# Optimization experiments

Hardware: AMD Instinct MI355X
Metric: run time of the kernel (lower is better)

Reference implementation:

```python
import jax, jax.numpy as jnp
import numpy as np

B, T, D = 4, 4096, 1024
HD = 64              # head_dim
H = D // HD          # n_heads = 16
C = 64               # chunk_size (T % C == 0)


def setup_inputs() -> dict:
    key = jax.random.key(0)
    k1, k2, k3 = jax.random.split(key, 3)
    out = jax.random.normal(k1, (B, T, D), jnp.float32)
    # Linear(d_model, d_model, bias=False) weights, ~1/sqrt(D) scale
    W_write = jax.random.normal(k2, (D, D), jnp.float32) * 0.03
    W_read = jax.random.normal(k3, (D, D), jnp.float32) * 0.03
    decay = jnp.full((H,), 4.6, jnp.float32)                 # torch init value
    log_alpha = jnp.log(jnp.full((H,), 0.03, jnp.float32))   # memory_alpha=0.03
    return {"out": out, "W_write": W_write, "W_read": W_read,
            "decay": decay, "log_alpha": log_alpha}


def reference(out, W_write, W_read, decay, log_alpha):
    Bb, Tt, Dd = out.shape
    d, Hh, Cc = HD, D // HD, C
    out32 = out.astype(jnp.float32)
    gamma = jax.nn.sigmoid(decay)          # (H,)
    log_gamma = jnp.log(gamma)

    # projections and head split: (B, H, T, d)
    v = (out32 @ W_write.T).reshape(Bb, Tt, Hh, d).transpose(0, 2, 1, 3)
    rk = out32.reshape(Bb, Tt, Hh, d).transpose(0, 2, 1, 3)
    wk = jnp.pad(rk[:, :, :-1], ((0, 0), (0, 0), (1, 0), (0, 0)))  # shift right by 1

    BH = Bb * Hh
    gamma_bh = jnp.tile(gamma, Bb)          # (BH,) index b*H+h -> gamma[h]
    log_gamma_bh = jnp.tile(log_gamma, Bb)
    nC = Tt // Cc
    # (nC, BH, C, d) so lax.scan runs over chunks
    v_ch = v.reshape(BH, nC, Cc, d).transpose(1, 0, 2, 3)
    rk_ch = rk.reshape(BH, nC, Cc, d).transpose(1, 0, 2, 3)
    wk_ch = wk.reshape(BH, nC, Cc, d).transpose(1, 0, 2, 3)

    p = jnp.arange(Cc)
    diffs = jnp.clip(p[:, None] - 1 - p[None, :], 0)          # (C, C)
    causal = p[:, None] > p[None, :]
    # per-(b,h) intra-chunk decay mask (BH, C, C)
    M = jnp.exp(diffs[None].astype(jnp.float32) * log_gamma_bh[:, None, None]) * causal[None]
    g_p = gamma_bh[:, None] ** p[None, :].astype(jnp.float32)            # (BH, C)
    g_w = gamma_bh[:, None] ** (Cc - 1 - p)[None, :].astype(jnp.float32)  # (BH, C)
    g_C = gamma_bh ** Cc                                                  # (BH,)

    def scan_fn(W, chunk):
        rk_c, wk_c, v_c = chunk                                   # each (BH, C, d)
        inter = jnp.einsum('bij,bcj->bci', W, rk_c) * g_p[:, :, None]
        S = jnp.einsum('bcd,bkd->bck', rk_c, wk_c)                # (BH, C, C)
        intra = jnp.einsum('bck,bkd->bcd', S * M, v_c)
        W_new = g_C[:, None, None] * W + jnp.einsum('bci,bcj->bij', v_c * g_w[:, :, None], wk_c)
        return W_new, inter + intra

    W0 = jnp.zeros((BH, d, d), jnp.float32)
    _, reads = jax.lax.scan(scan_fn, W0, (rk_ch, wk_ch, v_ch))   # (nC, BH, C, d)
    reads = reads.transpose(1, 0, 2, 3).reshape(Bb, Hh, Tt, d)
    alpha = jnp.exp(log_alpha)[None, :, None, None]
    reads = (alpha * reads).transpose(0, 2, 1, 3).reshape(Bb, Tt, Dd)
    return out + (reads @ W_read.T).astype(out.dtype)
```

## Files before the change

### kernel.cpp

```cpp
#include <hip/hip_runtime.h>
#include <hip/hip_bf16.h>
#include <stdint.h>


typedef __bf16 bf16x8 __attribute__((ext_vector_type(8)));
typedef float f32x4 __attribute__((ext_vector_type(4)));

#define GAS __attribute__((address_space(1)))
#define LAS __attribute__((address_space(3)))

__device__ __forceinline__ unsigned short f2bf(float f) {
  unsigned u = __float_as_uint(f);
  u = (u + 0x7fffu + ((u >> 16) & 1u)) >> 16;
  return (unsigned short)u;
}
__device__ __forceinline__ float bf2f(unsigned short h) {
  return __uint_as_float(((unsigned)h) << 16);
}

__global__ __launch_bounds__(256) void cast_f32_to_bf16(
    const float* __restrict__ src, unsigned short* __restrict__ dst, int n8) {
  int i = blockIdx.x * 256 + threadIdx.x;
  if (i >= n8) return;
  const float4* s = (const float4*)src + (size_t)i * 2;
  float4 f0 = s[0], f1 = s[1];
  union { uint4 u4; unsigned short us[8]; } o;
  o.us[0] = f2bf(f0.x); o.us[1] = f2bf(f0.y); o.us[2] = f2bf(f0.z); o.us[3] = f2bf(f0.w);
  o.us[4] = f2bf(f1.x); o.us[5] = f2bf(f1.y); o.us[6] = f2bf(f1.z); o.us[7] = f2bf(f1.w);
  ((uint4*)dst)[i] = o.u4;
}

__global__ __launch_bounds__(256) void cast_weights(
    const float* __restrict__ w1, const float* __restrict__ w2,
    unsigned short* __restrict__ dst) {
  int i = blockIdx.x * 256 + threadIdx.x;
  const float* src = (i < 131072) ? w1 : w2;
  int j = (i < 131072) ? i : i - 131072;
  const float4* s = (const float4*)src + (size_t)j * 2;
  float4 f0 = s[0], f1 = s[1];
  union { uint4 u4; unsigned short us[8]; } o;
  o.us[0] = f2bf(f0.x); o.us[1] = f2bf(f0.y); o.us[2] = f2bf(f0.z); o.us[3] = f2bf(f0.w);
  o.us[4] = f2bf(f1.x); o.us[5] = f2bf(f1.y); o.us[6] = f2bf(f1.z); o.us[7] = f2bf(f1.w);
  ((uint4*)dst)[i] = o.u4;
}

__device__ __forceinline__ void swizzle_bm_bn(int id, int& bm, int& bn) {
  int x = id & 7;
  int s = id >> 3;
  bn = s & 7;
  bm = ((s >> 3) << 3) | x;
}

__global__ __launch_bounds__(256, 4) void gemm_bt_bf16out(
    const unsigned short* __restrict__ A, const unsigned short* __restrict__ B,
    unsigned short* __restrict__ C, int M, int N, int K) {
  __shared__ unsigned short As[2][128 * 32];
  __shared__ unsigned short Bs[2][128 * 32];
  int tid = threadIdx.x;
  int l = tid & 63, w = tid >> 6;
  int bm, bn;
  swizzle_bm_bn(blockIdx.x, bm, bn);
  int wm = (w >> 1) * 64, wn = (w & 1) * 64;
  f32x4 acc[4][4];
#pragma unroll
  for (int mi = 0; mi < 4; mi++)
#pragma unroll
    for (int ni = 0; ni < 4; ni++) acc[mi][ni] = (f32x4){0.f, 0.f, 0.f, 0.f};
  const unsigned short* Ab = A + (size_t)bm * 128 * K;
  const unsigned short* Bb = B + (size_t)bn * 128 * K;
  int lr = l >> 2, lc = (l & 3) * 8;
  int lm = l & 15, q4 = l >> 4;
  const int nit = K >> 5;
#pragma unroll
  for (int q = 0; q < 2; q++) {
    int g = (w * 2 + q) * 16 + lr;
    __builtin_amdgcn_global_load_lds((GAS void*)(void*)(Ab + (size_t)g * K + lc),
                                     (LAS void*)(&As[0][(w * 2 + q) * 512]), 16, 0, 0);
    __builtin_amdgcn_global_load_lds((GAS void*)(void*)(Bb + (size_t)g * K + lc),
                                     (LAS void*)(&Bs[0][(w * 2 + q) * 512]), 16, 0, 0);
  }
  for (int it = 0; it < nit; it++) {
    __syncthreads();
    int buf = it & 1;
    if (it + 1 < nit) {
      int k0 = (it + 1) << 5;
#pragma unroll
      for (int q = 0; q < 2; q++) {
        int g = (w * 2 + q) * 16 + lr;
        __builtin_amdgcn_global_load_lds((GAS void*)(void*)(Ab + (size_t)g * K + k0 + lc),
                                         (LAS void*)(&As[buf ^ 1][(w * 2 + q) * 512]), 16, 0, 0);
        __builtin_amdgcn_global_load_lds((GAS void*)(void*)(Bb + (size_t)g * K + k0 + lc),
                                         (LAS void*)(&Bs[buf ^ 1][(w * 2 + q) * 512]), 16, 0, 0);
      }
    }
    bf16x8 a[4], b[4];
#pragma unroll
    for (int mi = 0; mi < 4; mi++) a[mi] = *(const bf16x8*)&As[buf][(wm + mi * 16 + lm) * 32 + q4 * 8];
#pragma unroll
    for (int ni = 0; ni < 4; ni++) b[ni] = *(const bf16x8*)&Bs[buf][(wn + ni * 16 + lm) * 32 + q4 * 8];
#pragma unroll
    for (int mi = 0; mi < 4; mi++)
#pragma unroll
      for (int ni = 0; ni < 4; ni++)
        acc[mi][ni] = __builtin_amdgcn_mfma_f32_16x16x32_bf16(a[mi], b[ni], acc[mi][ni], 0, 0, 0);
  }
#pragma unroll
  for (int mi = 0; mi < 4; mi++)
#pragma unroll
    for (int ni = 0; ni < 4; ni++) {
      int r0 = bm * 128 + wm + mi * 16 + q4 * 4;
      int col = bn * 128 + wn + ni * 16 + lm;
#pragma unroll
      for (int j = 0; j < 4; j++)
        C[(size_t)(r0 + j) * N + col] = f2bf(acc[mi][ni][j]);
    }
}

__global__ __launch_bounds__(256, 4) void gemm_bt_addout(
    const unsigned short* __restrict__ A, const unsigned short* __restrict__ B,
    const unsigned short* __restrict__ base_bf, float* __restrict__ C, int M, int N, int K) {
  __shared__ unsigned short As[2][128 * 32];
  __shared__ unsigned short Bs[2][128 * 32];
  int tid = threadIdx.x;
  int l = tid & 63, w = tid >> 6;
  int bm, bn;
  swizzle_bm_bn(blockIdx.x, bm, bn);
  int wm = (w >> 1) * 64, wn = (w & 1) * 64;
  int lr = l >> 2, lc = (l & 3) * 8;
  int lm = l & 15, q4 = l >> 4;
  f32x4 acc[4][4];
#pragma unroll
  for (int mi = 0; mi < 4; mi++)
#pragma unroll
    for (int ni = 0; ni < 4; ni++) {
      int r0 = bm * 128 + wm + mi * 16 + q4 * 4;
      int col = bn * 128 + wn + ni * 16 + lm;
#pragma unroll
      for (int j = 0; j < 4; j++)
        acc[mi][ni][j] = bf2f(base_bf[(size_t)(r0 + j) * N + col]);
    }
  const unsigned short* Ab = A + (size_t)bm * 128 * K;
  const unsigned short* Bb = B + (size_t)bn * 128 * K;
  const int nit = K >> 5;
#pragma unroll
  for (int q = 0; q < 2; q++) {
    int g = (w * 2 + q) * 16 + lr;
    __builtin_amdgcn_global_load_lds((GAS void*)(void*)(Ab + (size_t)g * K + lc),
                                     (LAS void*)(&As[0][(w * 2 + q) * 512]), 16, 0, 0);
    __builtin_amdgcn_global_load_lds((GAS void*)(void*)(Bb + (size_t)g * K + lc),
                                     (LAS void*)(&Bs[0][(w * 2 + q) * 512]), 16, 0, 0);
  }
  for (int it = 0; it < nit; it++) {
    __syncthreads();
    int buf = it & 1;
    if (it + 1 < nit) {
      int k0 = (it + 1) << 5;
#pragma unroll
      for (int q = 0; q < 2; q++) {
        int g = (w * 2 + q) * 16 + lr;
        __builtin_amdgcn_global_load_lds((GAS void*)(void*)(Ab + (size_t)g * K + k0 + lc),
                                         (LAS void*)(&As[buf ^ 1][(w * 2 + q) * 512]), 16, 0, 0);
        __builtin_amdgcn_global_load_lds((GAS void*)(void*)(Bb + (size_t)g * K + k0 + lc),
                                         (LAS void*)(&Bs[buf ^ 1][(w * 2 + q) * 512]), 16, 0, 0);
      }
    }
    bf16x8 a[4], b[4];
#pragma unroll
    for (int mi = 0; mi < 4; mi++) a[mi] = *(const bf16x8*)&As[buf][(wm + mi * 16 + lm) * 32 + q4 * 8];
#pragma unroll
    for (int ni = 0; ni < 4; ni++) b[ni] = *(const bf16x8*)&Bs[buf][(wn + ni * 16 + lm) * 32 + q4 * 8];
#pragma unroll
    for (int mi = 0; mi < 4; mi++)
#pragma unroll
      for (int ni = 0; ni < 4; ni++)
        acc[mi][ni] = __builtin_amdgcn_mfma_f32_16x16x32_bf16(a[mi], b[ni], acc[mi][ni], 0, 0, 0);
  }
#pragma unroll
  for (int mi = 0; mi < 4; mi++)
#pragma unroll
    for (int ni = 0; ni < 4; ni++) {
      int r0 = bm * 128 + wm + mi * 16 + q4 * 4;
      int col = bn * 128 + wn + ni * 16 + lm;
#pragma unroll
      for (int j = 0; j < 4; j++)
        C[(size_t)(r0 + j) * N + col] = acc[mi][ni][j];
    }
}

__global__ __launch_bounds__(256) void chunk_local(
    const unsigned short* __restrict__ rkg,
    const unsigned short* __restrict__ vg,
    const float* __restrict__ decay,
    unsigned short* __restrict__ intra_bf,
    unsigned short* __restrict__ U_bf) {
  int c = blockIdx.x, bh = blockIdx.y;
  int b = bh >> 4, h = bh & 15;
  int tid = threadIdx.x, l = tid & 63, w = tid >> 6;
  float gamma = 1.0f / (1.0f + __expf(-decay[h]));
  float lg = __logf(gamma);

  __shared__ unsigned short rk_s[64 * 72];
  __shared__ unsigned short wk_s[64 * 72];
  __shared__ unsigned short wkT_s[64 * 72];
  __shared__ unsigned short vT_s[64 * 72];
  __shared__ unsigned short S_s[64 * 72];

  const size_t rowbase = (((size_t)b * 4096 + (size_t)c * 64) * 1024) + h * 64;

#pragma unroll
  for (int r = 0; r < 2; r++) {
    int e = r * 256 + tid;
    int p = e >> 3, seg = e & 7;
    uint4 dr = *(const uint4*)(rkg + rowbase + (size_t)p * 1024 + seg * 8);
    *(uint4*)&rk_s[p * 72 + seg * 8] = dr;
    uint4 dv = *(const uint4*)(vg + rowbase + (size_t)p * 1024 + seg * 8);
    {
      unsigned uu[4] = {dv.x, dv.y, dv.z, dv.w};
#pragma unroll
      for (int qq = 0; qq < 4; qq++) {
        vT_s[(seg * 8 + qq * 2) * 72 + p] = (unsigned short)(uu[qq] & 0xffffu);
        vT_s[(seg * 8 + qq * 2 + 1) * 72 + p] = (unsigned short)(uu[qq] >> 16);
      }
    }
    int tg = c * 64 + p - 1;
    uint4 dw = make_uint4(0u, 0u, 0u, 0u);
    if (tg >= 0) dw = *(const uint4*)(rkg + ((size_t)b * 4096 + tg) * 1024 + h * 64 + seg * 8);
    *(uint4*)&wk_s[p * 72 + seg * 8] = dw;
    {
      unsigned uu[4] = {dw.x, dw.y, dw.z, dw.w};
#pragma unroll
      for (int qq = 0; qq < 4; qq++) {
        wkT_s[(seg * 8 + qq * 2) * 72 + p] = (unsigned short)(uu[qq] & 0xffffu);
        wkT_s[(seg * 8 + qq * 2 + 1) * 72 + p] = (unsigned short)(uu[qq] >> 16);
      }
    }
  }
  __syncthreads();

  int lm = l & 15, q4 = l >> 4;

  {
    bf16x8 a0 = *(const bf16x8*)&rk_s[(w * 16 + lm) * 72 + q4 * 8];
    bf16x8 a1 = *(const bf16x8*)&rk_s[(w * 16 + lm) * 72 + 32 + q4 * 8];
#pragma unroll
    for (int ni = 0; ni < 4; ni++) {
      bf16x8 b0 = *(const bf16x8*)&wk_s[(ni * 16 + lm) * 72 + q4 * 8];
      bf16x8 b1 = *(const bf16x8*)&wk_s[(ni * 16 + lm) * 72 + 32 + q4 * 8];
      f32x4 acc = {0.f, 0.f, 0.f, 0.f};
      acc = __builtin_amdgcn_mfma_f32_16x16x32_bf16(a0, b0, acc, 0, 0, 0);
      acc = __builtin_amdgcn_mfma_f32_16x16x32_bf16(a1, b1, acc, 0, 0, 0);
#pragma unroll
      for (int j = 0; j < 4; j++) {
        int p = w * 16 + q4 * 4 + j;
        int q = ni * 16 + lm;
        float m = (p > q) ? __expf(lg * (float)(p - 1 - q)) : 0.0f;
        S_s[p * 72 + q] = f2bf(acc[j] * m);
      }
    }
  }
  __syncthreads();

  {
    bf16x8 a0 = *(const bf16x8*)&S_s[(w * 16 + lm) * 72 + q4 * 8];
    bf16x8 a1 = *(const bf16x8*)&S_s[(w * 16 + lm) * 72 + 32 + q4 * 8];
#pragma unroll
    for (int ni = 0; ni < 4; ni++) {
      bf16x8 b0 = *(const bf16x8*)&vT_s[(ni * 16 + lm) * 72 + q4 * 8];
      bf16x8 b1 = *(const bf16x8*)&vT_s[(ni * 16 + lm) * 72 + 32 + q4 * 8];
      f32x4 acc = {0.f, 0.f, 0.f, 0.f};
      acc = __builtin_amdgcn_mfma_f32_16x16x32_bf16(a0, b0, acc, 0, 0, 0);
      acc = __builtin_amdgcn_mfma_f32_16x16x32_bf16(a1, b1, acc, 0, 0, 0);
#pragma unroll
      for (int j = 0; j < 4; j++) {
        int p = w * 16 + q4 * 4 + j;
        int i = ni * 16 + lm;
        intra_bf[rowbase + (size_t)p * 1024 + i] = f2bf(acc[j]);
      }
    }
  }

  {
    bf16x8 a0 = *(const bf16x8*)&vT_s[(w * 16 + lm) * 72 + q4 * 8];
    bf16x8 a1 = *(const bf16x8*)&vT_s[(w * 16 + lm) * 72 + 32 + q4 * 8];
#pragma unroll
    for (int jj = 0; jj < 8; jj++) {
      int p0 = q4 * 8 + jj;
      a0[jj] = (__bf16)((float)a0[jj] * __expf(lg * (float)(63 - p0)));
      a1[jj] = (__bf16)((float)a1[jj] * __expf(lg * (float)(63 - (p0 + 32))));
    }
    size_t ub = ((size_t)bh * 64 + c) * 4096;
#pragma unroll
    for (int nj = 0; nj < 4; nj++) {
      bf16x8 b0 = *(const bf16x8*)&wkT_s[(nj * 16 + lm) * 72 + q4 * 8];
      bf16x8 b1 = *(const bf16x8*)&wkT_s[(nj * 16 + lm) * 72 + 32 + q4 * 8];
      f32x4 acc = {0.f, 0.f, 0.f, 0.f};
      acc = __builtin_amdgcn_mfma_f32_16x16x32_bf16(a0, b0, acc, 0, 0, 0);
      acc = __builtin_amdgcn_mfma_f32_16x16x32_bf16(a1, b1, acc, 0, 0, 0);
#pragma unroll
      for (int j = 0; j < 4; j++) {
        int i = w * 16 + q4 * 4 + j;
        int col = nj * 16 + lm;
        U_bf[ub + i * 64 + col] = f2bf(acc[j]);
      }
    }
  }
}

__global__ __launch_bounds__(256) void scan_inter(
    const unsigned short* __restrict__ rkg, const unsigned short* __restrict__ U_bf,
    const unsigned short* __restrict__ intra_bf,
    const float* __restrict__ decay, const float* __restrict__ log_alpha,
    unsigned short* __restrict__ reads_bf) {
  int sp = blockIdx.x, bh = blockIdx.y;
  int b = bh >> 4, h = bh & 15;
  int tid = threadIdx.x, l = tid & 63, w = tid >> 6;
  int lm = l & 15, q4 = l >> 4;
  float gamma = 1.0f / (1.0f + __expf(-decay[h]));
  float lg = __logf(gamma);
  float gC = __expf(64.0f * lg);
  float alpha = __expf(log_alpha[h]);
  int i0 = sp * 16;

  __shared__ unsigned short rk_s[64 * 72];
  __shared__ unsigned short W_s[16 * 72];

  int lrow = tid >> 4, colb = (tid & 15) * 4;
  float Wreg[4] = {0.f, 0.f, 0.f, 0.f};

  int p_a = tid >> 3, seg_a = (tid & 7) * 8;
  const size_t bbase = (size_t)b * 4096 * 1024 + h * 64;
  size_t ubase = (size_t)bh * 64 * 4096;

  uint4 nrk0 = *(const uint4*)(rkg + bbase + (size_t)p_a * 1024 + seg_a);
  uint4 nrk1 = *(const uint4*)(rkg + bbase + (size_t)(p_a + 32) * 1024 + seg_a);
  ushort4 nu = *(const ushort4*)(U_bf + ubase + (i0 + lrow) * 64 + colb);

  for (int c = 0; c < 64; c++) {
    uint4 rk0 = nrk0, rk1 = nrk1;
    ushort4 uc = nu;
    __syncthreads();
    *(uint4*)&rk_s[p_a * 72 + seg_a] = rk0;
    *(uint4*)&rk_s[(p_a + 32) * 72 + seg_a] = rk1;
    {
      ushort4 wv;
      wv.x = f2bf(Wreg[0]); wv.y = f2bf(Wreg[1]); wv.z = f2bf(Wreg[2]); wv.w = f2bf(Wreg[3]);
      *(ushort4*)&W_s[lrow * 72 + colb] = wv;
    }
    __syncthreads();
    if (c + 1 < 64) {
      size_t nrb = bbase + (size_t)(c + 1) * 64 * 1024;
      nrk0 = *(const uint4*)(rkg + nrb + (size_t)p_a * 1024 + seg_a);
      nrk1 = *(const uint4*)(rkg + nrb + (size_t)(p_a + 32) * 1024 + seg_a);
      nu = *(const ushort4*)(U_bf + ubase + (size_t)(c + 1) * 4096 + (i0 + lrow) * 64 + colb);
    }
    f32x4 acc = {0.f, 0.f, 0.f, 0.f};
#pragma unroll
    for (int kst = 0; kst < 2; kst++) {
      bf16x8 a = *(const bf16x8*)&rk_s[(w * 16 + lm) * 72 + kst * 32 + q4 * 8];
      bf16x8 bb = *(const bf16x8*)&W_s[lm * 72 + kst * 32 + q4 * 8];
      acc = __builtin_amdgcn_mfma_f32_16x16x32_bf16(a, bb, acc, 0, 0, 0);
    }
    size_t rowbase = bbase + (size_t)c * 64 * 1024;
#pragma unroll
    for (int j = 0; j < 4; j++) {
      int ptok = w * 16 + q4 * 4 + j;
      float gp = __expf(lg * (float)ptok);
      size_t ad = rowbase + (size_t)ptok * 1024 + i0 + lm;
      reads_bf[ad] = f2bf(alpha * (acc[j] * gp + bf2f(intra_bf[ad])));
    }
    Wreg[0] = gC * Wreg[0] + bf2f(uc.x);
    Wreg[1] = gC * Wreg[1] + bf2f(uc.y);
    Wreg[2] = gC * Wreg[2] + bf2f(uc.z);
    Wreg[3] = gC * Wreg[3] + bf2f(uc.w);
  }
}

extern "C" void kernel_launch(void* const* d_in, const int* in_sizes, int n_in,
                              void* d_out, int out_size, void* d_ws, size_t ws_size,
                              hipStream_t stream) {
  const float* out_f = (const float*)d_in[0];
  const float* Ww = (const float*)d_in[1];
  const float* Wr = (const float*)d_in[2];
  const float* decay = (const float*)d_in[3];
  const float* lalpha = (const float*)d_in[4];

  char* ws = (char*)d_ws;
  unsigned short* outbf = (unsigned short*)(ws + 0);
  unsigned short* vbf   = (unsigned short*)(ws + 33554432);
  unsigned short* wwbf  = (unsigned short*)(ws + 67108864);
  unsigned short* wrbf  = (unsigned short*)(ws + 69206016);
  unsigned short* intra = (unsigned short*)(ws + 71303168);
  unsigned short* U     = (unsigned short*)(ws + 104857600);
  unsigned short* reads = (unsigned short*)(ws + 171966464);

  cast_f32_to_bf16<<<dim3(8192), 256, 0, stream>>>(out_f, outbf, 16777216 / 8);
  cast_weights<<<dim3(1024), 256, 0, stream>>>(Ww, Wr, wwbf);

  gemm_bt_bf16out<<<dim3(1024), 256, 0, stream>>>(outbf, wwbf, vbf, 16384, 1024, 1024);

  chunk_local<<<dim3(64, 64), 256, 0, stream>>>(outbf, vbf, decay, intra, U);
  scan_inter<<<dim3(4, 64), 256, 0, stream>>>(outbf, U, intra, decay, lalpha, reads);

  gemm_bt_addout<<<dim3(1024), 256, 0, stream>>>(reads, wrbf, outbf, (float*)d_out,
                                                 16384, 1024, 1024);
}
```

Before: 301.3 us.

## Split serial inter-chunk scan into state-scan and parallel per-chunk combine kernels

The old scan_inter kernel ran only 256 blocks, and each walked all 64 chunks serially, with syncthreads and a small MFMA at every step. The new code first runs a lightweight elementwise scan that writes the decayed state W for every chunk to workspace as bf16. A second kernel then launches one block per (chunk, bh) and computes rk·W plus the intra term fully in parallel. This exposes far more parallelism, at the cost of an extra 32MB write and read of per-chunk states and one more kernel launch.

```diff
diff --git a/kernel.cpp b/kernel.cpp
--- a/kernel.cpp
+++ b/kernel.cpp
@@ -306,72 +306,76 @@
   }
 }
 
-__global__ __launch_bounds__(256) void scan_inter(
-    const unsigned short* __restrict__ rkg, const unsigned short* __restrict__ U_bf,
+__global__ __launch_bounds__(256) void scan_w(
+    const unsigned short* __restrict__ U_bf, const float* __restrict__ decay,
+    unsigned short* __restrict__ Wst) {
+  int nsl = blockIdx.x, bh = blockIdx.y;
+  int h = bh & 15;
+  float gamma = 1.0f / (1.0f + __expf(-decay[h]));
+  float gC = __expf(64.0f * __logf(gamma));
+  int n0 = nsl * 512 + threadIdx.x * 2;
+  const unsigned short* Ub = U_bf + (size_t)bh * 64 * 4096 + n0;
+  unsigned short* Wb = Wst + (size_t)bh * 64 * 4096 + n0;
+  float w0 = 0.f, w1 = 0.f;
+#pragma unroll
+  for (int c = 0; c < 64; c++) {
+    unsigned u = *(const unsigned*)(Ub + (size_t)c * 4096);
+    ushort2 sv;
+    sv.x = f2bf(w0);
+    sv.y = f2bf(w1);
+    *(ushort2*)(Wb + (size_t)c * 4096) = sv;
+    w0 = gC * w0 + bf2f((unsigned short)(u & 0xffffu));
+    w1 = gC * w1 + bf2f((unsigned short)(u >> 16));
+  }
+}
+
+__global__ __launch_bounds__(256) void inter_combine(
+    const unsigned short* __restrict__ rkg, const unsigned short* __restrict__ Wst,
     const unsigned short* __restrict__ intra_bf,
     const float* __restrict__ decay, const float* __restrict__ log_alpha,
     unsigned short* __restrict__ reads_bf) {
-  int sp = blockIdx.x, bh = blockIdx.y;
+  int c = blockIdx.x, bh = blockIdx.y;
   int b = bh >> 4, h = bh & 15;
   int tid = threadIdx.x, l = tid & 63, w = tid >> 6;
   int lm = l & 15, q4 = l >> 4;
   float gamma = 1.0f / (1.0f + __expf(-decay[h]));
   float lg = __logf(gamma);
-  float gC = __expf(64.0f * lg);
   float alpha = __expf(log_alpha[h]);
-  int i0 = sp * 16;
 
   __shared__ unsigned short rk_s[64 * 72];
-  __shared__ unsigned short W_s[16 * 72];
-
-  int lrow = tid >> 4, colb = (tid & 15) * 4;
-  float Wreg[4] = {0.f, 0.f, 0.f, 0.f};
-
-  int p_a = tid >> 3, seg_a = (tid & 7) * 8;
-  const size_t bbase = (size_t)b * 4096 * 1024 + h * 64;
-  size_t ubase = (size_t)bh * 64 * 4096;
-
-  uint4 nrk0 = *(const uint4*)(rkg + bbase + (size_t)p_a * 1024 + seg_a);
-  uint4 nrk1 = *(const uint4*)(rkg + bbase + (size_t)(p_a + 32) * 1024 + seg_a);
-  ushort4 nu = *(const ushort4*)(U_bf + ubase + (i0 + lrow) * 64 + colb);
-
-  for (int c = 0; c < 64; c++) {
-    uint4 rk0 = nrk0, rk1 = nrk1;
-    ushort4 uc = nu;
-    __syncthreads();
-    *(uint4*)&rk_s[p_a * 72 + seg_a] = rk0;
-    *(uint4*)&rk_s[(p_a + 32) * 72 + seg_a] = rk1;
-    {
-      ushort4 wv;
-      wv.x = f2bf(Wreg[0]); wv.y = f2bf(Wreg[1]); wv.z = f2bf(Wreg[2]); wv.w = f2bf(Wreg[3]);
-      *(ushort4*)&W_s[lrow * 72 + colb] = wv;
-    }
-    __syncthreads();
-    if (c + 1 < 64) {
-      size_t nrb = bbase + (size_t)(c + 1) * 64 * 1024;
-      nrk0 = *(const uint4*)(rkg + nrb + (size_t)p_a * 1024 + seg_a);
-      nrk1 = *(const uint4*)(rkg + nrb + (size_t)(p_a + 32) * 1024 + seg_a);
-      nu = *(const ushort4*)(U_bf + ubase + (size_t)(c + 1) * 4096 + (i0 + lrow) * 64 + colb);
-    }
+  __shared__ unsigned short W_s[64 * 72];
+  __shared__ unsigned short in_s[64 * 72];
+
+  const size_t rowbase = (((size_t)b * 4096 + (size_t)c * 64) * 1024) + h * 64;
+  const size_t wbase = ((size_t)bh * 64 + c) * 4096;
+
+#pragma unroll
+  for (int r = 0; r < 2; r++) {
+    int e = r * 256 + tid;
+    int p = e >> 3, seg = (e & 7) * 8;
+    *(uint4*)&rk_s[p * 72 + seg] = *(const uint4*)(rkg + rowbase + (size_t)p * 1024 + seg);
+    *(uint4*)&in_s[p * 72 + seg] = *(const uint4*)(intra_bf + rowbase + (size_t)p * 1024 + seg);
+    *(uint4*)&W_s[p * 72 + seg] = *(const uint4*)(Wst + wbase + (size_t)p * 64 + seg);
+  }
+  __syncthreads();
+
+  bf16x8 a0 = *(const bf16x8*)&rk_s[(w * 16 + lm) * 72 + q4 * 8];
+  bf16x8 a1 = *(const bf16x8*)&rk_s[(w * 16 + lm) * 72 + 32 + q4 * 8];
+#pragma unroll
+  for (int ni = 0; ni < 4; ni++) {
+    bf16x8 b0 = *(const bf16x8*)&W_s[(ni * 16 + lm) * 72 + q4 * 8];
+    bf16x8 b1 = *(const bf16x8*)&W_s[(ni * 16 + lm) * 72 + 32 + q4 * 8];
     f32x4 acc = {0.f, 0.f, 0.f, 0.f};
-#pragma unroll
-    for (int kst = 0; kst < 2; kst++) {
-      bf16x8 a = *(const bf16x8*)&rk_s[(w * 16 + lm) * 72 + kst * 32 + q4 * 8];
-      bf16x8 bb = *(const bf16x8*)&W_s[lm * 72 + kst * 32 + q4 * 8];
-      acc = __builtin_amdgcn_mfma_f32_16x16x32_bf16(a, bb, acc, 0, 0, 0);
-    }
-    size_t rowbase = bbase + (size_t)c * 64 * 1024;
+    acc = __builtin_amdgcn_mfma_f32_16x16x32_bf16(a0, b0, acc, 0, 0, 0);
+    acc = __builtin_amdgcn_mfma_f32_16x16x32_bf16(a1, b1, acc, 0, 0, 0);
 #pragma unroll
     for (int j = 0; j < 4; j++) {
-      int ptok = w * 16 + q4 * 4 + j;
-      float gp = __expf(lg * (float)ptok);
-      size_t ad = rowbase + (size_t)ptok * 1024 + i0 + lm;
-      reads_bf[ad] = f2bf(alpha * (acc[j] * gp + bf2f(intra_bf[ad])));
-    }
-    Wreg[0] = gC * Wreg[0] + bf2f(uc.x);
-    Wreg[1] = gC * Wreg[1] + bf2f(uc.y);
-    Wreg[2] = gC * Wreg[2] + bf2f(uc.z);
-    Wreg[3] = gC * Wreg[3] + bf2f(uc.w);
+      int p = w * 16 + q4 * 4 + j;
+      int i = ni * 16 + lm;
+      float gp = __expf(lg * (float)p);
+      reads_bf[rowbase + (size_t)p * 1024 + i] =
+          f2bf(alpha * (acc[j] * gp + bf2f(in_s[p * 72 + i])));
+    }
   }
 }
 
@@ -391,6 +395,7 @@
   unsigned short* wrbf  = (unsigned short*)(ws + 69206016);
   unsigned short* intra = (unsigned short*)(ws + 71303168);
   unsigned short* U     = (unsigned short*)(ws + 104857600);
+  unsigned short* Wst   = (unsigned short*)(ws + 138412032);
   unsigned short* reads = (unsigned short*)(ws + 171966464);
 
   cast_f32_to_bf16<<<dim3(8192), 256, 0, stream>>>(out_f, outbf, 16777216 / 8);
@@ -399,7 +404,9 @@
   gemm_bt_bf16out<<<dim3(1024), 256, 0, stream>>>(outbf, wwbf, vbf, 16384, 1024, 1024);
 
   chunk_local<<<dim3(64, 64), 256, 0, stream>>>(outbf, vbf, decay, intra, U);
-  scan_inter<<<dim3(4, 64), 256, 0, stream>>>(outbf, U, intra, decay, lalpha, reads);
+
+  scan_w<<<dim3(8, 64), 256, 0, stream>>>(U, decay, Wst);
+  inter_combine<<<dim3(64, 64), 256, 0, stream>>>(outbf, Wst, intra, decay, lalpha, reads);
 
   gemm_bt_addout<<<dim3(1024), 256, 0, stream>>>(reads, wrbf, outbf, (float*)d_out,
                                                  16384, 1024, 1024);
```

Result: faster. 288.0 us (-4.4%).
